# Kernel optimization log

Measured on AMD Instinct MI355X. Metric: run time of the kernel, lower is better.

Reference implementation:

```python
import jax, jax.numpy as jnp
import numpy as np

N, D, P = 8192, 512, 3
TEMP, SIM_TH, DIS_TH, CLIP = 0.1, 0.15, 0.35, 30.0
NEG = -1e9  # finite stand-in for -inf mask (exp underflows to 0 identically)


def setup_inputs() -> dict:
    key = jax.random.key(0)
    k1, k2 = jax.random.split(key)
    embeddings = jax.random.normal(k1, (N, D), dtype=jnp.float32)
    thetas = jax.random.uniform(k2, (N, P), dtype=jnp.float32)
    return {"embeddings": embeddings, "thetas": thetas}


def reference(embeddings, thetas):
    n = embeddings.shape[0]
    # F.normalize(dim=-1)
    e = embeddings / jnp.maximum(
        jnp.linalg.norm(embeddings, axis=-1, keepdims=True), 1e-12)
    sim = jnp.clip(e @ e.T / TEMP, -CLIP, CLIP)  # [N, N]

    # cdist(thetas, thetas) normalized by its max; only feeds boolean masks
    t = jax.lax.stop_gradient(thetas)
    sq = jnp.sum(t * t, axis=1)
    d2 = jnp.maximum(sq[:, None] + sq[None, :] - 2.0 * (t @ t.T), 0.0)
    dist = jnp.sqrt(d2)
    dist = dist / (dist.max() + 1e-8)

    eye = jnp.eye(n, dtype=bool)
    pos = (dist < SIM_TH) & ~eye      # positives (self excluded: diag is -inf masked)
    neg = dist > DIS_TH               # negatives (diag never included: dist==0)
    sel = pos | neg

    # per-row cross_entropy over logits [pos_idx; neg_idx] with label 0 is:
    #   -sim[i, first_pos_index(i)] + logsumexp_{j in sel(i)} sim[i, j]
    masked = jnp.where(sel, sim, NEG)
    denom = jax.nn.logsumexp(masked, axis=1)            # [N]
    tgt = jnp.argmax(pos, axis=1)                       # first positive index
    tgt_logit = jnp.take_along_axis(sim, tgt[:, None], axis=1)[:, 0]
    valid = pos.any(axis=1) & neg.any(axis=1)
    per_row = jnp.where(valid, denom - tgt_logit, 0.0)
    cnt = valid.sum()
    return jnp.where(cnt > 0, per_row.sum() / jnp.maximum(cnt, 1), 0.0)
```

## Files before the change

### kernel.cpp

```cpp
#include <hip/hip_runtime.h>

#define N 8192
#define D 512

typedef __attribute__((ext_vector_type(8))) short short8;
typedef __attribute__((ext_vector_type(4))) float f32x4;

typedef const __attribute__((address_space(1))) unsigned int* gas_t;
typedef __attribute__((address_space(3))) unsigned int* las_t;

static __device__ __forceinline__ unsigned short f2bf(float f) {
    unsigned u = __float_as_uint(f);
    unsigned r = (u + 0x7FFFu + ((u >> 16) & 1u)) >> 16;
    return (unsigned short)r;
}
static __device__ __forceinline__ float bf2f(unsigned u) {
    return __uint_as_float(u << 16);
}
static __device__ __forceinline__ void gl_lds16(const unsigned short* g, char* l) {
    __builtin_amdgcn_global_load_lds((gas_t)g, (las_t)l, 16, 0, 0);
}
static __device__ __forceinline__ int tri_cum(int r) { return r * (129 - r) / 2; }

__global__ void knorm(const float* __restrict__ emb, unsigned short* __restrict__ e,
                      const float* __restrict__ th, float4* __restrict__ th4,
                      float* __restrict__ srow, unsigned* __restrict__ jminrow,
                      unsigned* __restrict__ negrow, unsigned* __restrict__ d2mb) {
    int row  = blockIdx.x * 4 + (threadIdx.x >> 6);
    int lane = threadIdx.x & 63;
    const float4* src = (const float4*)(emb + (size_t)row * D);
    float4 v0 = src[lane * 2];
    float4 v1 = src[lane * 2 + 1];
    float ss = v0.x*v0.x + v0.y*v0.y + v0.z*v0.z + v0.w*v0.w
             + v1.x*v1.x + v1.y*v1.y + v1.z*v1.z + v1.w*v1.w;
#pragma unroll
    for (int off = 1; off < 64; off <<= 1) ss += __shfl_xor(ss, off, 64);
    float inv = 1.0f / fmaxf(sqrtf(ss), 1e-12f);
    unsigned short h0 = f2bf(v0.x * inv), h1 = f2bf(v0.y * inv);
    unsigned short h2 = f2bf(v0.z * inv), h3 = f2bf(v0.w * inv);
    unsigned short h4 = f2bf(v1.x * inv), h5 = f2bf(v1.y * inv);
    unsigned short h6 = f2bf(v1.z * inv), h7 = f2bf(v1.w * inv);
    uint4 pk;
    pk.x = (unsigned)h0 | ((unsigned)h1 << 16);
    pk.y = (unsigned)h2 | ((unsigned)h3 << 16);
    pk.z = (unsigned)h4 | ((unsigned)h5 << 16);
    pk.w = (unsigned)h6 | ((unsigned)h7 << 16);
    ((uint4*)(e + (size_t)row * D))[lane] = pk;

    int tid = threadIdx.x;
    if (tid < 4) {
        int i = blockIdx.x * 4 + tid;
        float x = th[3 * i], y = th[3 * i + 1], z = th[3 * i + 2];
        float4 v; v.x = x; v.y = y; v.z = z; v.w = x * x + y * y + z * z;
        th4[i] = v;
        srow[i] = 0.0f;
        jminrow[i] = 0xFFFFFFFFu;
        negrow[i] = 0u;
    }
    if (blockIdx.x == 0 && tid == 0) *d2mb = 0u;
}

__global__ void kd2max(const float4* __restrict__ th4, unsigned* __restrict__ d2mb) {
    int widx = blockIdx.x * 4 + (threadIdx.x >> 6);
    int lane = threadIdx.x & 63;
    float4 t1 = th4[widx];
    int i2 = N - 1 - widx;
    float4 t2 = th4[i2];
    float m = 0.0f;
#pragma unroll 4
    for (int j = widx + 1 + lane; j < N; j += 64) {
        float4 tj = th4[j];
        float dot = t1.x * tj.x + t1.y * tj.y + t1.z * tj.z;
        m = fmaxf(m, t1.w + tj.w - 2.0f * dot);
    }
#pragma unroll 4
    for (int j = i2 + 1 + lane; j < N; j += 64) {
        float4 tj = th4[j];
        float dot = t2.x * tj.x + t2.y * tj.y + t2.z * tj.z;
        m = fmaxf(m, t2.w + tj.w - 2.0f * dot);
    }
#pragma unroll
    for (int off = 1; off < 64; off <<= 1) m = fmaxf(m, __shfl_xor(m, off, 64));
    __shared__ float red[4];
    int w = threadIdx.x >> 6;
    if (lane == 0) red[w] = m;
    __syncthreads();
    if (threadIdx.x == 0) {
        m = fmaxf(fmaxf(red[0], red[1]), fmaxf(red[2], red[3]));
        atomicMax(d2mb, __float_as_uint(m));
    }
}

__global__ __launch_bounds__(256) void kmain(
    const unsigned short* __restrict__ e, const float4* __restrict__ th4,
    const unsigned* __restrict__ d2mb, float* __restrict__ srow,
    unsigned* __restrict__ jminrow, unsigned* __restrict__ negrow) {
    __shared__ __align__(16) char sA0[16384];
    __shared__ __align__(16) char sB0[16384];
    __shared__ __align__(16) char sA1[16384];
    __shared__ __align__(16) char sB1[16384];

    const int tid  = threadIdx.x;
    const int lane = tid & 63;
    const int w    = tid >> 6;
    const int wr   = w >> 1;
    const int wc   = w & 1;

    const int bid = (int)blockIdx.x;
    const int swz = (bid & 7) * 260 + (bid >> 3);
    int rb = (int)((129.0f - sqrtf(16641.0f - 8.0f * (float)swz)) * 0.5f);
    rb = rb < 0 ? 0 : (rb > 63 ? 63 : rb);
    while (tri_cum(rb + 1) <= swz) rb++;
    while (tri_cum(rb) > swz) rb--;
    const int cb = rb + (swz - tri_cum(rb));
    const bool isdiag = (rb == cb);
    const int r0 = rb * 128, c0 = cb * 128;

    const int l8 = lane >> 3, l7 = lane & 7;
    const int srcoff = ((l7 ^ l8) << 3);
    const unsigned short* pA[4];
    const unsigned short* pB[4];
#pragma unroll
    for (int cc = 0; cc < 4; cc++) {
        const int c = w * 4 + cc;
        pA[cc] = e + (size_t)(r0 + 8 * c + l8) * D + srcoff;
        pB[cc] = e + (size_t)(c0 + 8 * c + l8) * D + srcoff;
    }

    const int fr = lane & 15;
    const int fq = lane >> 4;

    f32x4 acc[4][4];
#pragma unroll
    for (int mt = 0; mt < 4; mt++)
#pragma unroll
        for (int nt = 0; nt < 4; nt++) acc[mt][nt] = (f32x4){0.f, 0.f, 0.f, 0.f};

    auto stage = [&](char* dA, char* dB, int k0) {
#pragma unroll
        for (int cc = 0; cc < 4; cc++) {
            gl_lds16(pA[cc] + k0, dA + (w * 4 + cc) * 1024);
            gl_lds16(pB[cc] + k0, dB + (w * 4 + cc) * 1024);
        }
    };
    auto compute = [&](const char* cA, const char* cB) {
#pragma unroll
        for (int ks = 0; ks < 2; ++ks) {
            const int kb = ((ks << 6) | (fq << 4)) ^ (l7 << 4);
            short8 a[4], b[4];
#pragma unroll
            for (int mt = 0; mt < 4; mt++)
                a[mt] = *(const short8*)(cA + (wr * 64 + mt * 16 + fr) * 128 + kb);
#pragma unroll
            for (int nt = 0; nt < 4; nt++)
                b[nt] = *(const short8*)(cB + (wc * 64 + nt * 16 + fr) * 128 + kb);
#pragma unroll
            for (int mt = 0; mt < 4; mt++)
#pragma unroll
                for (int nt = 0; nt < 4; nt++)
                    acc[mt][nt] = __builtin_amdgcn_mfma_f32_16x16x32_bf16(
                        a[mt], b[nt], acc[mt][nt], 0, 0, 0);
        }
    };

    stage(sA0, sB0, 0);
    asm volatile("s_waitcnt vmcnt(0)" ::: "memory");
    __builtin_amdgcn_s_barrier();
#pragma unroll
    for (int kt = 0; kt < 8; kt += 2) {
        stage(sA1, sB1, (kt + 1) * 64);
        compute(sA0, sB0);
        asm volatile("s_waitcnt vmcnt(0)" ::: "memory");
        __builtin_amdgcn_s_barrier();
        if (kt + 2 < 8) stage(sA0, sB0, (kt + 2) * 64);
        compute(sA1, sB1);
        asm volatile("s_waitcnt vmcnt(0)" ::: "memory");
        __builtin_amdgcn_s_barrier();
    }

    const float dmax = sqrtf(__uint_as_float(*d2mb)) + 1e-8f;
    const float p2 = 0.0225f * dmax * dmax;
    const float n2 = 0.1225f * dmax * dmax;

    const int j0 = c0 + wc * 64 + fr;
    float4 thj[4];
#pragma unroll
    for (int nt = 0; nt < 4; nt++) thj[nt] = th4[j0 + nt * 16];

    float*    lds_rs = (float*)sA0;
    unsigned* lds_rj = (unsigned*)(sA0 + 1024);
    unsigned* lds_rn = (unsigned*)(sA0 + 2048);
    float*    lds_cs = (float*)(sA0 + 3072);
    unsigned* lds_cj = (unsigned*)(sA0 + 4096);
    unsigned* lds_cn = (unsigned*)(sA0 + 5120);

    float    csum[4]; unsigned cjm[4], cng[4];
#pragma unroll
    for (int nt = 0; nt < 4; nt++) { csum[nt] = 0.0f; cjm[nt] = 0xFFFFFFFFu; cng[nt] = 0u; }

    const float K_EXP = 14.4269504089f;

    const int i0 = r0 + wr * 64 + fq * 4;
#pragma unroll
    for (int mt = 0; mt < 4; mt++) {
#pragma unroll
        for (int rr = 0; rr < 4; rr++) {
            const int i = i0 + mt * 16 + rr;
            const float4 ti = th4[i];
            float sv = 0.0f; unsigned jv = 0xFFFFFFFFu, nv = 0u;
#pragma unroll
            for (int nt = 0; nt < 4; nt++) {
                const int j = j0 + nt * 16;
                const float4 tj = thj[nt];
                float dot = ti.x * tj.x + ti.y * tj.y + ti.z * tj.z;
                float d2 = fmaf(-2.0f, dot, ti.w + tj.w);
                bool pos = isdiag ? ((d2 < p2) && (j != i)) : (d2 < p2);
                bool neg = (d2 > n2);
                float c = (pos || neg) ? exp2f(acc[mt][nt][rr] * K_EXP) : 0.0f;
                sv += c;
                if (neg) nv = 1u;
                if (pos) jv = min(jv, (unsigned)j);
                if (!isdiag) {
                    csum[nt] += c;
                    if (neg) cng[nt] = 1u;
                    if (pos) cjm[nt] = min(cjm[nt], (unsigned)i);
                }
            }
#pragma unroll
            for (int off = 1; off < 16; off <<= 1) {
                sv += __shfl_xor(sv, off, 64);
                jv = min(jv, (unsigned)__shfl_xor((int)jv, off, 64));
                nv |= (unsigned)__shfl_xor((int)nv, off, 64);
            }
            if (fr == 0) {
                const int rl = wr * 64 + mt * 16 + fq * 4 + rr;
                lds_rs[wc * 128 + rl] = sv;
                lds_rj[wc * 128 + rl] = jv;
                lds_rn[wc * 128 + rl] = nv;
            }
        }
    }

    if (!isdiag) {
#pragma unroll
        for (int nt = 0; nt < 4; nt++) {
            float sv = csum[nt]; unsigned jv = cjm[nt], nv = cng[nt];
#pragma unroll
            for (int off = 16; off < 64; off <<= 1) {
                sv += __shfl_xor(sv, off, 64);
                jv = min(jv, (unsigned)__shfl_xor((int)jv, off, 64));
                nv |= (unsigned)__shfl_xor((int)nv, off, 64);
            }
            if (fq == 0) {
                const int cl = wc * 64 + nt * 16 + fr;
                lds_cs[wr * 128 + cl] = sv;
                lds_cj[wr * 128 + cl] = jv;
                lds_cn[wr * 128 + cl] = nv;
            }
        }
    }
    __syncthreads();
    if (tid < 128) {
        float    sv = lds_rs[tid] + lds_rs[128 + tid];
        unsigned jv = min(lds_rj[tid], lds_rj[128 + tid]);
        unsigned nv = lds_rn[tid] | lds_rn[128 + tid];
        atomicAdd(&srow[r0 + tid], sv);
        atomicMin(&jminrow[r0 + tid], jv);
        atomicOr(&negrow[r0 + tid], nv);
        if (!isdiag) {
            float    cv = lds_cs[tid] + lds_cs[128 + tid];
            unsigned cj = min(lds_cj[tid], lds_cj[128 + tid]);
            unsigned cn = lds_cn[tid] | lds_cn[128 + tid];
            atomicAdd(&srow[c0 + tid], cv);
            atomicMin(&jminrow[c0 + tid], cj);
            atomicOr(&negrow[c0 + tid], cn);
        }
    }
}

__global__ void krow(const unsigned short* __restrict__ e, const float* __restrict__ srow,
                     const unsigned* __restrict__ jminrow, const unsigned* __restrict__ negrow,
                     float* __restrict__ pr, float* __restrict__ vf) {
    int row  = blockIdx.x * 4 + (threadIdx.x >> 6);
    int lane = threadIdx.x & 63;
    unsigned jmv = jminrow[row];
    bool valid = (jmv != 0xFFFFFFFFu) && (negrow[row] != 0u);
    float p = 0.0f;
    if (valid) {
        const uint4* a = (const uint4*)(e + (size_t)row * D);
        const uint4* b = (const uint4*)(e + (size_t)jmv * D);
        uint4 va = a[lane], vb = b[lane];
        float dot = 0.0f;
        dot += bf2f(va.x & 0xFFFFu) * bf2f(vb.x & 0xFFFFu);
        dot += bf2f(va.x >> 16)     * bf2f(vb.x >> 16);
        dot += bf2f(va.y & 0xFFFFu) * bf2f(vb.y & 0xFFFFu);
        dot += bf2f(va.y >> 16)     * bf2f(vb.y >> 16);
        dot += bf2f(va.z & 0xFFFFu) * bf2f(vb.z & 0xFFFFu);
        dot += bf2f(va.z >> 16)     * bf2f(vb.z >> 16);
        dot += bf2f(va.w & 0xFFFFu) * bf2f(vb.w & 0xFFFFu);
        dot += bf2f(va.w >> 16)     * bf2f(vb.w >> 16);
#pragma unroll
        for (int off = 1; off < 64; off <<= 1) dot += __shfl_xor(dot, off, 64);
        p = logf(srow[row]) - dot * 10.0f;
    }
    if (lane == 0) { pr[row] = p; vf[row] = valid ? 1.0f : 0.0f; }
}

__global__ void kfinal(const float* __restrict__ pr, const float* __restrict__ vf,
                       float* __restrict__ out) {
    __shared__ float ls[1024];
    __shared__ float lc[1024];
    int t = threadIdx.x;
    float sv = 0.0f, cv = 0.0f;
#pragma unroll
    for (int k = 0; k < 8; k++) { sv += pr[t * 8 + k]; cv += vf[t * 8 + k]; }
    ls[t] = sv; lc[t] = cv;
    __syncthreads();
    for (int off = 512; off > 0; off >>= 1) {
        if (t < off) { ls[t] += ls[t + off]; lc[t] += lc[t + off]; }
        __syncthreads();
    }
    if (t == 0) out[0] = (lc[0] > 0.0f) ? (ls[0] / lc[0]) : 0.0f;
}

extern "C" void kernel_launch(void* const* d_in, const int* in_sizes, int n_in,
                              void* d_out, int out_size, void* d_ws, size_t ws_size,
                              hipStream_t stream) {
    const float* emb = (const float*)d_in[0];
    const float* th  = (const float*)d_in[1];
    float* out = (float*)d_out;
    char* ws = (char*)d_ws;

    unsigned short* e    = (unsigned short*)(ws);
    float4*   th4        = (float4*)(ws + 8388608);
    float*    srow       = (float*)(ws + 8519680);
    unsigned* jminr      = (unsigned*)(ws + 8552448);
    unsigned* negr       = (unsigned*)(ws + 8585216);
    float*    pr         = (float*)(ws + 8617984);
    float*    vf         = (float*)(ws + 8650752);
    unsigned* d2mb       = (unsigned*)(ws + 8683520);

    knorm<<<N / 4, 256, 0, stream>>>(emb, e, th, th4, srow, jminr, negr, d2mb);
    kd2max<<<1024, 256, 0, stream>>>(th4, d2mb);
    kmain<<<2080, 256, 0, stream>>>(e, th4, d2mb, srow, jminr, negr);
    krow<<<N / 4, 256, 0, stream>>>(e, srow, jminr, negr, pr, vf);
    kfinal<<<1, 1024, 0, stream>>>(pr, vf, out);
}
```

Measured before the change: 134.2 us.

## Split main GEMM tile across eight waves and register-block the max-distance kernel

The main kernel now runs 512 threads per block in a 2x4 wave grid. Each wave computes a 64x32 sub-tile instead of 64x64, so more waves share the same 128x128 tile and LDS buffers, which should hide latency better and lower per-wave register pressure. The cross-wave row reduction widens from two to four partials, and the LDS scratch offsets are adjusted to fit. Separately, the max-distance kernel has each wave handle four rows per sweep, reusing each loaded theta vector four times, and launches a quarter as many blocks. The risk is that the tighter launch bounds force register spills and that shorter per-wave MFMA chains weaken instruction-level parallelism.

```diff
diff --git a/kernel.cpp b/kernel.cpp
--- a/kernel.cpp
+++ b/kernel.cpp
@@ -63,21 +63,26 @@
 __global__ void kd2max(const float4* __restrict__ th4, unsigned* __restrict__ d2mb) {
     int widx = blockIdx.x * 4 + (threadIdx.x >> 6);
     int lane = threadIdx.x & 63;
-    float4 t1 = th4[widx];
-    int i2 = N - 1 - widx;
-    float4 t2 = th4[i2];
+    int q0 = widx * 4;
+    int m0 = N - 4 - q0;
+    float4 a0 = th4[q0], a1 = th4[q0 + 1], a2 = th4[q0 + 2], a3 = th4[q0 + 3];
+    float4 b0 = th4[m0], b1 = th4[m0 + 1], b2 = th4[m0 + 2], b3 = th4[m0 + 3];
     float m = 0.0f;
-#pragma unroll 4
-    for (int j = widx + 1 + lane; j < N; j += 64) {
+    for (int j = q0 + 1 + lane; j < N; j += 64) {
         float4 tj = th4[j];
-        float dot = t1.x * tj.x + t1.y * tj.y + t1.z * tj.z;
-        m = fmaxf(m, t1.w + tj.w - 2.0f * dot);
-    }
-#pragma unroll 4
-    for (int j = i2 + 1 + lane; j < N; j += 64) {
+        float d;
+        d = a0.w + tj.w - 2.0f * (a0.x*tj.x + a0.y*tj.y + a0.z*tj.z); m = fmaxf(m, d);
+        d = a1.w + tj.w - 2.0f * (a1.x*tj.x + a1.y*tj.y + a1.z*tj.z); m = fmaxf(m, d);
+        d = a2.w + tj.w - 2.0f * (a2.x*tj.x + a2.y*tj.y + a2.z*tj.z); m = fmaxf(m, d);
+        d = a3.w + tj.w - 2.0f * (a3.x*tj.x + a3.y*tj.y + a3.z*tj.z); m = fmaxf(m, d);
+    }
+    for (int j = m0 + 1 + lane; j < N; j += 64) {
         float4 tj = th4[j];
-        float dot = t2.x * tj.x + t2.y * tj.y + t2.z * tj.z;
-        m = fmaxf(m, t2.w + tj.w - 2.0f * dot);
+        float d;
+        d = b0.w + tj.w - 2.0f * (b0.x*tj.x + b0.y*tj.y + b0.z*tj.z); m = fmaxf(m, d);
+        d = b1.w + tj.w - 2.0f * (b1.x*tj.x + b1.y*tj.y + b1.z*tj.z); m = fmaxf(m, d);
+        d = b2.w + tj.w - 2.0f * (b2.x*tj.x + b2.y*tj.y + b2.z*tj.z); m = fmaxf(m, d);
+        d = b3.w + tj.w - 2.0f * (b3.x*tj.x + b3.y*tj.y + b3.z*tj.z); m = fmaxf(m, d);
     }
 #pragma unroll
     for (int off = 1; off < 64; off <<= 1) m = fmaxf(m, __shfl_xor(m, off, 64));
@@ -91,7 +96,7 @@
     }
 }
 
-__global__ __launch_bounds__(256) void kmain(
+__global__ __launch_bounds__(512, 4) void kmain(
     const unsigned short* __restrict__ e, const float4* __restrict__ th4,
     const unsigned* __restrict__ d2mb, float* __restrict__ srow,
     unsigned* __restrict__ jminrow, unsigned* __restrict__ negrow) {
@@ -103,8 +108,8 @@
     const int tid  = threadIdx.x;
     const int lane = tid & 63;
     const int w    = tid >> 6;
-    const int wr   = w >> 1;
-    const int wc   = w & 1;
+    const int wr   = w >> 2;
+    const int wc   = w & 3;
 
     const int bid = (int)blockIdx.x;
     const int swz = (bid & 7) * 260 + (bid >> 3);
@@ -118,11 +123,11 @@
 
     const int l8 = lane >> 3, l7 = lane & 7;
     const int srcoff = ((l7 ^ l8) << 3);
-    const unsigned short* pA[4];
-    const unsigned short* pB[4];
-#pragma unroll
-    for (int cc = 0; cc < 4; cc++) {
-        const int c = w * 4 + cc;
+    const unsigned short* pA[2];
+    const unsigned short* pB[2];
+#pragma unroll
+    for (int cc = 0; cc < 2; cc++) {
+        const int c = w * 2 + cc;
         pA[cc] = e + (size_t)(r0 + 8 * c + l8) * D + srcoff;
         pB[cc] = e + (size_t)(c0 + 8 * c + l8) * D + srcoff;
     }
@@ -130,34 +135,34 @@
     const int fr = lane & 15;
     const int fq = lane >> 4;
 
-    f32x4 acc[4][4];
+    f32x4 acc[4][2];
 #pragma unroll
     for (int mt = 0; mt < 4; mt++)
 #pragma unroll
-        for (int nt = 0; nt < 4; nt++) acc[mt][nt] = (f32x4){0.f, 0.f, 0.f, 0.f};
+        for (int nt = 0; nt < 2; nt++) acc[mt][nt] = (f32x4){0.f, 0.f, 0.f, 0.f};
 
     auto stage = [&](char* dA, char* dB, int k0) {
 #pragma unroll
-        for (int cc = 0; cc < 4; cc++) {
-            gl_lds16(pA[cc] + k0, dA + (w * 4 + cc) * 1024);
-            gl_lds16(pB[cc] + k0, dB + (w * 4 + cc) * 1024);
+        for (int cc = 0; cc < 2; cc++) {
+            gl_lds16(pA[cc] + k0, dA + (w * 2 + cc) * 1024);
+            gl_lds16(pB[cc] + k0, dB + (w * 2 + cc) * 1024);
         }
     };
     auto compute = [&](const char* cA, const char* cB) {
 #pragma unroll
         for (int ks = 0; ks < 2; ++ks) {
             const int kb = ((ks << 6) | (fq << 4)) ^ (l7 << 4);
-            short8 a[4], b[4];
+            short8 a[4], b[2];
 #pragma unroll
             for (int mt = 0; mt < 4; mt++)
                 a[mt] = *(const short8*)(cA + (wr * 64 + mt * 16 + fr) * 128 + kb);
 #pragma unroll
-            for (int nt = 0; nt < 4; nt++)
-                b[nt] = *(const short8*)(cB + (wc * 64 + nt * 16 + fr) * 128 + kb);
+            for (int nt = 0; nt < 2; nt++)
+                b[nt] = *(const short8*)(cB + (wc * 32 + nt * 16 + fr) * 128 + kb);
 #pragma unroll
             for (int mt = 0; mt < 4; mt++)
 #pragma unroll
-                for (int nt = 0; nt < 4; nt++)
+                for (int nt = 0; nt < 2; nt++)
                     acc[mt][nt] = __builtin_amdgcn_mfma_f32_16x16x32_bf16(
                         a[mt], b[nt], acc[mt][nt], 0, 0, 0);
         }
@@ -182,21 +187,21 @@
     const float p2 = 0.0225f * dmax * dmax;
     const float n2 = 0.1225f * dmax * dmax;
 
-    const int j0 = c0 + wc * 64 + fr;
-    float4 thj[4];
-#pragma unroll
-    for (int nt = 0; nt < 4; nt++) thj[nt] = th4[j0 + nt * 16];
+    const int j0 = c0 + wc * 32 + fr;
+    float4 thj[2];
+#pragma unroll
+    for (int nt = 0; nt < 2; nt++) thj[nt] = th4[j0 + nt * 16];
 
     float*    lds_rs = (float*)sA0;
-    unsigned* lds_rj = (unsigned*)(sA0 + 1024);
-    unsigned* lds_rn = (unsigned*)(sA0 + 2048);
-    float*    lds_cs = (float*)(sA0 + 3072);
-    unsigned* lds_cj = (unsigned*)(sA0 + 4096);
-    unsigned* lds_cn = (unsigned*)(sA0 + 5120);
-
-    float    csum[4]; unsigned cjm[4], cng[4];
-#pragma unroll
-    for (int nt = 0; nt < 4; nt++) { csum[nt] = 0.0f; cjm[nt] = 0xFFFFFFFFu; cng[nt] = 0u; }
+    unsigned* lds_rj = (unsigned*)(sA0 + 2048);
+    unsigned* lds_rn = (unsigned*)(sA0 + 4096);
+    float*    lds_cs = (float*)(sA0 + 6144);
+    unsigned* lds_cj = (unsigned*)(sA0 + 7168);
+    unsigned* lds_cn = (unsigned*)(sA0 + 8192);
+
+    float    csum[2]; unsigned cjm[2], cng[2];
+#pragma unroll
+    for (int nt = 0; nt < 2; nt++) { csum[nt] = 0.0f; cjm[nt] = 0xFFFFFFFFu; cng[nt] = 0u; }
 
     const float K_EXP = 14.4269504089f;
 
@@ -209,7 +214,7 @@
             const float4 ti = th4[i];
             float sv = 0.0f; unsigned jv = 0xFFFFFFFFu, nv = 0u;
 #pragma unroll
-            for (int nt = 0; nt < 4; nt++) {
+            for (int nt = 0; nt < 2; nt++) {
                 const int j = j0 + nt * 16;
                 const float4 tj = thj[nt];
                 float dot = ti.x * tj.x + ti.y * tj.y + ti.z * tj.z;
@@ -243,7 +248,7 @@
 
     if (!isdiag) {
 #pragma unroll
-        for (int nt = 0; nt < 4; nt++) {
+        for (int nt = 0; nt < 2; nt++) {
             float sv = csum[nt]; unsigned jv = cjm[nt], nv = cng[nt];
 #pragma unroll
             for (int off = 16; off < 64; off <<= 1) {
@@ -252,7 +257,7 @@
                 nv |= (unsigned)__shfl_xor((int)nv, off, 64);
             }
             if (fq == 0) {
-                const int cl = wc * 64 + nt * 16 + fr;
+                const int cl = wc * 32 + nt * 16 + fr;
                 lds_cs[wr * 128 + cl] = sv;
                 lds_cj[wr * 128 + cl] = jv;
                 lds_cn[wr * 128 + cl] = nv;
@@ -261,9 +266,10 @@
     }
     __syncthreads();
     if (tid < 128) {
-        float    sv = lds_rs[tid] + lds_rs[128 + tid];
-        unsigned jv = min(lds_rj[tid], lds_rj[128 + tid]);
-        unsigned nv = lds_rn[tid] | lds_rn[128 + tid];
+        float    sv = lds_rs[tid] + lds_rs[128 + tid] + lds_rs[256 + tid] + lds_rs[384 + tid];
+        unsigned jv = min(min(lds_rj[tid], lds_rj[128 + tid]),
+                          min(lds_rj[256 + tid], lds_rj[384 + tid]));
+        unsigned nv = lds_rn[tid] | lds_rn[128 + tid] | lds_rn[256 + tid] | lds_rn[384 + tid];
         atomicAdd(&srow[r0 + tid], sv);
         atomicMin(&jminrow[r0 + tid], jv);
         atomicOr(&negrow[r0 + tid], nv);
@@ -341,8 +347,8 @@
     unsigned* d2mb       = (unsigned*)(ws + 8683520);
 
     knorm<<<N / 4, 256, 0, stream>>>(emb, e, th, th4, srow, jminr, negr, d2mb);
-    kd2max<<<1024, 256, 0, stream>>>(th4, d2mb);
-    kmain<<<2080, 256, 0, stream>>>(e, th4, d2mb, srow, jminr, negr);
+    kd2max<<<256, 256, 0, stream>>>(th4, d2mb);
+    kmain<<<2080, 512, 0, stream>>>(e, th4, d2mb, srow, jminr, negr);
     krow<<<N / 4, 256, 0, stream>>>(e, srow, jminr, negr, pr, vf);
     kfinal<<<1, 1024, 0, stream>>>(pr, vf, out);
 }
```

Result: slower. 148.4 us (+10.6%).
